# Kernel tuning notes

Hardware: AMD Instinct MI355X
Metric: run time of the kernel (lower is better)

Reference implementation:

```python
import jax, jax.numpy as jnp
import numpy as np

H = 1024  # hidden_dims

def _gru_scan(xs, h0, wih, whh, bih, bhh):
    # xs: (T, D_in); torch GRU gate order: r, z, n
    xp = xs @ wih.T + bih  # (T, 3H), precomputed input projection
    def step(h, xp_t):
        hh = h @ whh.T + bhh
        r = jax.nn.sigmoid(xp_t[:H] + hh[:H])
        z = jax.nn.sigmoid(xp_t[H:2 * H] + hh[H:2 * H])
        n = jnp.tanh(xp_t[2 * H:] + r * hh[2 * H:])
        h_new = (1.0 - z) * n + z * h
        return h_new, None
    h_last, _ = jax.lax.scan(step, h0, xp)
    return h_last

def _lstm_step(h_in, wih, bih, bhh):
    # single-step nn.LSTM(H, H) with zero initial (h0, c0): Whh terms vanish, biases remain.
    # torch LSTM gate order: i, f, g, o
    xp = h_in @ wih.T + bih + bhh  # (4H,)
    i = jax.nn.sigmoid(xp[:H])
    g = jnp.tanh(xp[2 * H:3 * H])
    o = jax.nn.sigmoid(xp[3 * H:])
    c = i * g  # f * c0 == 0
    return o * jnp.tanh(c)

def setup_inputs() -> dict:
    key = jax.random.key(0)
    ks = jax.random.split(key, 20)
    T, D_w, D_i = 8192, 32, 32
    s = 0.05
    inp = {
        "weather_window": jax.random.normal(ks[0], (T, 1, D_w), jnp.float32),
        "infect_window": jax.random.normal(ks[1], (T, 1, D_i), jnp.float32),
        "time_window": jax.random.uniform(ks[2], (T, 1), jnp.float32),
        "h_init": jax.random.normal(ks[3], (1, 1, H), jnp.float32),
        "enc_w1": jax.random.normal(ks[4], (512, 64), jnp.float32) * s,
        "enc_b1": jax.random.normal(ks[5], (512,), jnp.float32) * s,
        "enc_w2": jax.random.normal(ks[6], (1024, 512), jnp.float32) * s,
        "enc_b2": jax.random.normal(ks[7], (1024,), jnp.float32) * s,
        "gru_wih": jax.random.normal(ks[8], (3 * H, H), jnp.float32) * s,
        "gru_whh": jax.random.normal(ks[9], (3 * H, H), jnp.float32) * s,
        "gru_bih": jax.random.normal(ks[10], (3 * H,), jnp.float32) * s,
        "gru_bhh": jax.random.normal(ks[11], (3 * H,), jnp.float32) * s,
        "lstm_wih": jax.random.normal(ks[12], (4 * H, H), jnp.float32) * s,
        "lstm_bih": jax.random.normal(ks[13], (4 * H,), jnp.float32) * s,
        "lstm_bhh": jax.random.normal(ks[14], (4 * H,), jnp.float32) * s,
        "dec_w1": jax.random.normal(ks[15], (512, 1024), jnp.float32) * s,
        "dec_b1": jax.random.normal(ks[16], (512,), jnp.float32) * s,
        "dec_w2": jax.random.normal(ks[17], (8, 512), jnp.float32) * s,
        "dec_b2": jax.random.normal(ks[18], (8,), jnp.float32) * s,
    }
    return inp

def reference(weather_window, infect_window, time_window, h_init,
              enc_w1, enc_b1, enc_w2, enc_b2,
              gru_wih, gru_whh, gru_bih, gru_bhh,
              lstm_wih, lstm_bih, lstm_bhh,
              dec_w1, dec_b1, dec_w2, dec_b2):
    T = weather_window.shape[0]
    # use_diff_time = False branch
    data_window = jnp.concatenate([weather_window, infect_window], axis=2)  # (T,1,64)
    rev = data_window[::-1]  # flip(0)
    # Encoder FC stack
    x = jax.nn.relu(rev @ enc_w1.T + enc_b1)
    x = jax.nn.relu(x @ enc_w2.T + enc_b2)  # (T,1,H)
    # Encoder GRU -> final hidden state
    h_enc = _gru_scan(x[:, 0, :], h_init[0, 0], gru_wih, gru_whh, gru_bih, gru_bhh)  # (H,)
    def step(h, _):
        h_new = _lstm_step(h, lstm_wih, lstm_bih, lstm_bhh)
        return h_new, h_new
    _, hs_tail = jax.lax.scan(step, h_enc, None, length=T - 1)  # (T-1, H)
    hs = jnp.concatenate([h_enc[None, :], hs_tail], axis=0)  # (T, H)
    hs = hs[:, None, None, :]  # (T,1,1,H), matches torch.stack of (1,1,H)
    # Decoder FC stack
    y = jax.nn.relu(hs @ dec_w1.T + dec_b1)
    y = y @ dec_w2.T + dec_b2  # (T,1,1,8)
    return y
```

## Files before the change

kernel.cpp:

```cpp
#include <hip/hip_runtime.h>
#include <hip/hip_bf16.h>
#include <math.h>

#define T_STEPS 8192
#define HDIM    1024
#define GW      128
#define NSLOT   512

#define OFF_REV   ((size_t)0)
#define OFF_X1    ((size_t)2097152)
#define OFF_B     ((size_t)18874368)
#define OFF_C     ((size_t)52428800)
#define WS_NEEDED ((size_t)153092096)

typedef float f4 __attribute__((ext_vector_type(4)));

__device__ inline float sigm(float x)   { return 1.0f / (1.0f + __expf(-x)); }
__device__ inline float tanh_f(float x) { float e = __expf(2.0f * x); return 1.0f - 2.0f / (e + 1.0f); }

__device__ inline void store_cohr(f4* p, f4 v) {
    asm volatile("global_store_dwordx4 %0, %1, off sc0 sc1"
                 :: "v"(p), "v"(v) : "memory");
}

__device__ inline void poll_pair(const f4* p, unsigned want, f4& a, f4& b) {
    for (;;) {
        f4 va, vb;
        asm volatile("global_load_dwordx4 %0, %2, off sc0 sc1\n\t"
                     "global_load_dwordx4 %1, %2, off offset:16 sc0 sc1\n\t"
                     "s_waitcnt vmcnt(0)"
                     : "=&v"(va), "=&v"(vb) : "v"(p) : "memory");
        if (__float_as_uint(va.w) == want && __float_as_uint(vb.w) == want) {
            a = va; b = vb; return;
        }
        __builtin_amdgcn_s_sleep(1);
    }
}

__global__ void build_rev(const float* __restrict__ wea, const float* __restrict__ inf,
                          float* __restrict__ rev) {
    int idx = blockIdx.x * blockDim.x + threadIdx.x;
    if (idx >= T_STEPS * 64) return;
    int t = idx >> 6, c = idx & 63;
    int ts = T_STEPS - 1 - t;
    rev[idx] = (c < 32) ? wea[ts * 32 + c] : inf[ts * 32 + (c - 32)];
}

__global__ void seed_slots(const float* __restrict__ h0, f4* __restrict__ slots) {
    int i = blockIdx.x * blockDim.x + threadIdx.x;
    if (i < NSLOT) {
        f4 v;
        v.x = h0[2 * i]; v.y = h0[2 * i + 1]; v.z = 0.0f;
        v.w = __uint_as_float(0u);
        store_cohr(&slots[i], v);
    }
}

__global__ __launch_bounds__(256) void gemm_bias_act(
    const float* __restrict__ A, const float* __restrict__ W,
    const float* __restrict__ bias, float* __restrict__ C,
    int M, int N, int K, int relu)
{
    __shared__ float As[32][68];
    __shared__ float Ws[32][68];
    const int tid = threadIdx.x;
    const int tx = tid & 15, ty = tid >> 4;
    const int bm = blockIdx.y, bn = blockIdx.x;
    const float* Ab = A + (size_t)bm * 64 * K;
    const float* Wb = W + (size_t)bn * 64 * K;
    float acc[4][4] = {};

    for (int k0 = 0; k0 < K; k0 += 32) {
#pragma unroll
        for (int q = 0; q < 2; ++q) {
            int idx = tid * 2 + q;
            int row = idx >> 3;
            int kc  = (idx & 7) << 2;
            float4 av = *(const float4*)(Ab + (size_t)row * K + k0 + kc);
            As[kc + 0][row] = av.x; As[kc + 1][row] = av.y;
            As[kc + 2][row] = av.z; As[kc + 3][row] = av.w;
            float4 wv = *(const float4*)(Wb + (size_t)row * K + k0 + kc);
            Ws[kc + 0][row] = wv.x; Ws[kc + 1][row] = wv.y;
            Ws[kc + 2][row] = wv.z; Ws[kc + 3][row] = wv.w;
        }
        __syncthreads();
#pragma unroll
        for (int k = 0; k < 32; ++k) {
            float4 a = *(const float4*)&As[k][ty << 2];
            float4 b = *(const float4*)&Ws[k][tx << 2];
            acc[0][0] += a.x*b.x; acc[0][1] += a.x*b.y; acc[0][2] += a.x*b.z; acc[0][3] += a.x*b.w;
            acc[1][0] += a.y*b.x; acc[1][1] += a.y*b.y; acc[1][2] += a.y*b.z; acc[1][3] += a.y*b.w;
            acc[2][0] += a.z*b.x; acc[2][1] += a.z*b.y; acc[2][2] += a.z*b.z; acc[2][3] += a.z*b.w;
            acc[3][0] += a.w*b.x; acc[3][1] += a.w*b.y; acc[3][2] += a.w*b.z; acc[3][3] += a.w*b.w;
        }
        __syncthreads();
    }

    int m0 = bm * 64 + (ty << 2), n0 = bn * 64 + (tx << 2);
    float4 bv = *(const float4*)(bias + n0);
#pragma unroll
    for (int r = 0; r < 4; ++r) {
        float4 o;
        o.x = acc[r][0] + bv.x; o.y = acc[r][1] + bv.y;
        o.z = acc[r][2] + bv.z; o.w = acc[r][3] + bv.w;
        if (relu) {
            o.x = fmaxf(o.x, 0.f); o.y = fmaxf(o.y, 0.f);
            o.z = fmaxf(o.z, 0.f); o.w = fmaxf(o.w, 0.f);
        }
        *(float4*)(C + (size_t)(m0 + r) * N + n0) = o;
    }
}

__global__ __launch_bounds__(256, 1) void gru_scan(
    const float* __restrict__ whh,
    const float* __restrict__ bhh,
    const float* __restrict__ xp,
    f4* __restrict__ slots,
    float* __restrict__ hs)
{
    __shared__ float h_sh[2][HDIM];
    const int g = blockIdx.x, tid = threadIdx.x;
    const int w = tid >> 6, l = tid & 63;
    const int wv = g * 4 + w;
    const int iA = 2 * wv, iB = iA + 1;
    const int rows[6] = { iA, HDIM + iA, 2*HDIM + iA, iB, HDIM + iB, 2*HDIM + iB };

    f4 Wf[6][4];
#pragma unroll
    for (int r = 0; r < 6; ++r) {
        const float* wr = whh + (size_t)rows[r] * HDIM + 4 * l;
#pragma unroll
        for (int j = 0; j < 4; ++j) Wf[r][j] = *(const f4*)(wr + 256 * j);
    }
#pragma unroll
    for (int r = 0; r < 6; ++r)
#pragma unroll
        for (int j = 0; j < 4; ++j)
            asm volatile("" : "+v"(Wf[r][j]));

    float b0 = 0.f, b1 = 0.f, b2 = 0.f;
    float xv0 = 0.f, xv1 = 0.f, xv2 = 0.f;
    int xrow = (l == 0) ? iA : iB;
    if (l < 2) {
        b0 = bhh[xrow]; b1 = bhh[HDIM + xrow]; b2 = bhh[2*HDIM + xrow];
        xv0 = xp[xrow]; xv1 = xp[HDIM + xrow]; xv2 = xp[2*HDIM + xrow];
    }

    for (int t = 0; t < T_STEPS; ++t) {
        const int buf = t & 1;
        f4 sa, sb;
        poll_pair(slots + (size_t)buf * NSLOT + 2 * tid, (unsigned)t, sa, sb);
        h_sh[buf][4*tid + 0] = sa.x; h_sh[buf][4*tid + 1] = sa.y;
        h_sh[buf][4*tid + 2] = sb.x; h_sh[buf][4*tid + 3] = sb.y;
        __syncthreads();

        f4 h4[4];
#pragma unroll
        for (int j = 0; j < 4; ++j) h4[j] = *(const f4*)&h_sh[buf][256*j + 4*l];

        float red[6];
#pragma unroll
        for (int r = 0; r < 6; ++r) {
            f4 p = Wf[r][0]*h4[0] + Wf[r][1]*h4[1] + Wf[r][2]*h4[2] + Wf[r][3]*h4[3];
            float v = p.x + p.y + p.z + p.w;
#pragma unroll
            for (int off = 32; off > 0; off >>= 1) v += __shfl_xor(v, off, 64);
            red[r] = v;
        }

        float hn = 0.f;
        if (l < 2) {
            float rd0 = (l == 0) ? red[0] : red[3];
            float rd1 = (l == 0) ? red[1] : red[4];
            float rd2 = (l == 0) ? red[2] : red[5];
            float hh_r = rd0 + b0, hh_z = rd1 + b1, hh_n = rd2 + b2;
            float r_ = sigm(xv0 + hh_r);
            float z_ = sigm(xv1 + hh_z);
            float n_ = tanh_f(xv2 + r_ * hh_n);
            float hp = h_sh[buf][xrow];
            hn = (1.0f - z_) * n_ + z_ * hp;
        }
        float hBv = __shfl(hn, 1, 64);
        if (l == 0) {
            unsigned pub = (unsigned)(t + 1);
            f4 s; s.x = hn; s.y = hBv; s.z = 0.0f; s.w = __uint_as_float(pub);
            store_cohr(slots + (size_t)(pub & 1) * NSLOT + wv, s);
            if (t == T_STEPS - 1) { hs[iA] = hn; hs[iB] = hBv; }
        }
        if (l < 2 && t + 1 < T_STEPS) {
            const float* xq = xp + (size_t)(t + 1) * (3 * HDIM);
            xv0 = xq[xrow]; xv1 = xq[HDIM + xrow]; xv2 = xq[2*HDIM + xrow];
        }
    }
}

__global__ __launch_bounds__(256, 1) void lstm_scan(
    const float* __restrict__ wih,
    const float* __restrict__ bih,
    const float* __restrict__ bhh,
    f4* __restrict__ slots,
    float* __restrict__ hs)
{
    __shared__ float h_sh[2][HDIM];
    __shared__ int eqf[4];
    const int g = blockIdx.x, tid = threadIdx.x;
    const int w = tid >> 6, l = tid & 63;
    const int wv = g * 4 + w;
    const int iA = 2 * wv, iB = iA + 1;
    const int rows[6] = { iA, 2*HDIM + iA, 3*HDIM + iA, iB, 2*HDIM + iB, 3*HDIM + iB };

    f4 Wf[6][4];
#pragma unroll
    for (int r = 0; r < 6; ++r) {
        const float* wr = wih + (size_t)rows[r] * HDIM + 4 * l;
#pragma unroll
        for (int j = 0; j < 4; ++j) Wf[r][j] = *(const f4*)(wr + 256 * j);
    }
#pragma unroll
    for (int r = 0; r < 6; ++r)
#pragma unroll
        for (int j = 0; j < 4; ++j)
            asm volatile("" : "+v"(Wf[r][j]));

    float b0 = 0.f, b1 = 0.f, b2 = 0.f;
    int xrow = (l == 0) ? iA : iB;
    if (l < 2) {
        b0 = bih[xrow]          + bhh[xrow];
        b1 = bih[2*HDIM + xrow] + bhh[2*HDIM + xrow];
        b2 = bih[3*HDIM + xrow] + bhh[3*HDIM + xrow];
    }

    unsigned pax = 0u, pay = 0u, pbx = 0u, pby = 0u;

    for (int s = 1; s < T_STEPS; ++s) {
        const unsigned want = (unsigned)(8191 + s);
        const unsigned pub  = (unsigned)(8192 + s);
        const int buf = (int)(want & 1);
        f4 sa, sb;
        poll_pair(slots + (size_t)buf * NSLOT + 2 * tid, want, sa, sb);

        bool eq = (s > 1)
               && (__float_as_uint(sa.x) == pax) && (__float_as_uint(sa.y) == pay)
               && (__float_as_uint(sb.x) == pbx) && (__float_as_uint(sb.y) == pby);
        unsigned long long bm = __ballot(eq);
        if (l == 0) eqf[w] = (bm == ~0ull) ? 1 : 0;
        pax = __float_as_uint(sa.x); pay = __float_as_uint(sa.y);
        pbx = __float_as_uint(sb.x); pby = __float_as_uint(sb.y);

        h_sh[buf][4*tid + 0] = sa.x; h_sh[buf][4*tid + 1] = sa.y;
        h_sh[buf][4*tid + 2] = sb.x; h_sh[buf][4*tid + 3] = sb.y;
        __syncthreads();

        if (eqf[0] & eqf[1] & eqf[2] & eqf[3]) {
            float4 hv = make_float4(sa.x, sa.y, sb.x, sb.y);
            for (int k = s + g; k < T_STEPS; k += GW)
                *(float4*)&hs[(size_t)k * HDIM + 4 * tid] = hv;
            return;
        }

        f4 h4[4];
#pragma unroll
        for (int j = 0; j < 4; ++j) h4[j] = *(const f4*)&h_sh[buf][256*j + 4*l];

        float red[6];
#pragma unroll
        for (int r = 0; r < 6; ++r) {
            f4 p = Wf[r][0]*h4[0] + Wf[r][1]*h4[1] + Wf[r][2]*h4[2] + Wf[r][3]*h4[3];
            float v = p.x + p.y + p.z + p.w;
#pragma unroll
            for (int off = 32; off > 0; off >>= 1) v += __shfl_xor(v, off, 64);
            red[r] = v;
        }

        float hn = 0.f;
        if (l < 2) {
            float rd0 = (l == 0) ? red[0] : red[3];
            float rd1 = (l == 0) ? red[1] : red[4];
            float rd2 = (l == 0) ? red[2] : red[5];
            float i_ = sigm(rd0 + b0);
            float g_ = tanh_f(rd1 + b1);
            float o_ = sigm(rd2 + b2);
            hn = o_ * tanh_f(i_ * g_);
        }
        float hBv = __shfl(hn, 1, 64);
        if (l == 0) {
            f4 sv; sv.x = hn; sv.y = hBv; sv.z = 0.0f; sv.w = __uint_as_float(pub);
            store_cohr(slots + (size_t)(pub & 1) * NSLOT + wv, sv);
            hs[(size_t)s * HDIM + iA] = hn;
            hs[(size_t)s * HDIM + iB] = hBv;
        }
    }
}

__global__ __launch_bounds__(256) void dec2_kernel(
    const float* __restrict__ y1,
    const float* __restrict__ w2,
    const float* __restrict__ b2,
    float* __restrict__ out)
{
    const int w = threadIdx.x >> 6, l = threadIdx.x & 63;
    const int t = blockIdx.x * 4 + w;
    const float* yr = y1 + (size_t)t * 512;
    float yv[8];
#pragma unroll
    for (int j = 0; j < 8; ++j) yv[j] = yr[l + 64 * j];
    float o[8];
#pragma unroll
    for (int n = 0; n < 8; ++n) {
        const float* wr = w2 + n * 512;
        float s = 0.f;
#pragma unroll
        for (int j = 0; j < 8; ++j) s += yv[j] * wr[l + 64 * j];
#pragma unroll
        for (int off = 32; off > 0; off >>= 1) s += __shfl_xor(s, off, 64);
        o[n] = s;
    }
    if (l == 0) {
#pragma unroll
        for (int n = 0; n < 8; ++n) out[(size_t)t * 8 + n] = o[n] + b2[n];
    }
}

extern "C" void kernel_launch(void* const* d_in, const int* in_sizes, int n_in,
                              void* d_out, int out_size, void* d_ws, size_t ws_size,
                              hipStream_t stream)
{
    const float* wea      = (const float*)d_in[0];
    const float* inf      = (const float*)d_in[1];
    const float* h_init   = (const float*)d_in[3];
    const float* enc_w1   = (const float*)d_in[4];
    const float* enc_b1   = (const float*)d_in[5];
    const float* enc_w2   = (const float*)d_in[6];
    const float* enc_b2   = (const float*)d_in[7];
    const float* gru_wih  = (const float*)d_in[8];
    const float* gru_whh  = (const float*)d_in[9];
    const float* gru_bih  = (const float*)d_in[10];
    const float* gru_bhh  = (const float*)d_in[11];
    const float* lstm_wih = (const float*)d_in[12];
    const float* lstm_bih = (const float*)d_in[13];
    const float* lstm_bhh = (const float*)d_in[14];
    const float* dec_w1   = (const float*)d_in[15];
    const float* dec_b1   = (const float*)d_in[16];
    const float* dec_w2   = (const float*)d_in[17];
    const float* dec_b2   = (const float*)d_in[18];

    if (ws_size < WS_NEEDED) return;

    char* ws = (char*)d_ws;
    float* rev   = (float*)(ws + OFF_REV);
    float* x1    = (float*)(ws + OFF_X1);
    float* x2    = (float*)(ws + OFF_B);
    float* hs    = (float*)(ws + OFF_B);
    float* xp    = (float*)(ws + OFF_C);
    float* y1    = (float*)(ws + OFF_C);
    f4*    slots = (f4*)(ws + OFF_X1);

    build_rev<<<(T_STEPS * 64) / 256, 256, 0, stream>>>(wea, inf, rev);

    gemm_bias_act<<<dim3(8, 128), 256, 0, stream>>>(rev, enc_w1, enc_b1, x1,
                                                    T_STEPS, 512, 64, 1);
    gemm_bias_act<<<dim3(16, 128), 256, 0, stream>>>(x1, enc_w2, enc_b2, x2,
                                                     T_STEPS, 1024, 512, 1);
    gemm_bias_act<<<dim3(48, 128), 256, 0, stream>>>(x2, gru_wih, gru_bih, xp,
                                                     T_STEPS, 3 * HDIM, HDIM, 0);
    seed_slots<<<2, 256, 0, stream>>>(h_init, slots);
    gru_scan<<<GW, 256, 0, stream>>>(gru_whh, gru_bhh, xp, slots, hs);
    lstm_scan<<<GW, 256, 0, stream>>>(lstm_wih, lstm_bih, lstm_bhh, slots, hs);

    gemm_bias_act<<<dim3(8, 128), 256, 0, stream>>>(hs, dec_w1, dec_b1, y1,
                                                    T_STEPS, 512, HDIM, 1);
    dec2_kernel<<<T_STEPS / 4, 256, 0, stream>>>(y1, dec_w2, dec_b2, (float*)d_out);
}
```

Baseline: 43.09 ms.

## Detect periodic LSTM orbits with Brent-style anchors and replicate the cycle

The existing early exit only fires when the autoregressive hidden state becomes an exact fixed point. This change compares each new state against an anchor state that is reset at power-of-two steps, so an exact cycle of any period can be detected. Once a cycle is found, the remaining timesteps are filled by copying the earlier cycle entries from hs instead of running the serial recurrence. It also drops the s_sleep from the polling loop to cut per-step handoff latency. It writes hs with coherent stores and adds a fixed delay before the copy so other blocks' stores are visible. The cost is more spinning pressure on memory, plus reliance on those coherence assumptions when reading back hs.

```diff
diff --git a/kernel.cpp b/kernel.cpp
--- a/kernel.cpp
+++ b/kernel.cpp
@@ -14,12 +14,23 @@
 #define WS_NEEDED ((size_t)153092096)
 
 typedef float f4 __attribute__((ext_vector_type(4)));
+typedef float f2v __attribute__((ext_vector_type(2)));
 
 __device__ inline float sigm(float x)   { return 1.0f / (1.0f + __expf(-x)); }
 __device__ inline float tanh_f(float x) { float e = __expf(2.0f * x); return 1.0f - 2.0f / (e + 1.0f); }
 
+__device__ inline f4 load_cohr(const f4* p) {
+    f4 v;
+    asm volatile("global_load_dwordx4 %0, %1, off sc0 sc1\n\ts_waitcnt vmcnt(0)"
+                 : "=v"(v) : "v"(p) : "memory");
+    return v;
+}
 __device__ inline void store_cohr(f4* p, f4 v) {
     asm volatile("global_store_dwordx4 %0, %1, off sc0 sc1"
+                 :: "v"(p), "v"(v) : "memory");
+}
+__device__ inline void store_cohr8(f2v* p, f2v v) {
+    asm volatile("global_store_dwordx2 %0, %1, off sc0 sc1"
                  :: "v"(p), "v"(v) : "memory");
 }
 
@@ -33,7 +44,6 @@
         if (__float_as_uint(va.w) == want && __float_as_uint(vb.w) == want) {
             a = va; b = vb; return;
         }
-        __builtin_amdgcn_s_sleep(1);
     }
 }
 
@@ -230,7 +240,8 @@
         b2 = bih[3*HDIM + xrow] + bhh[3*HDIM + xrow];
     }
 
-    unsigned pax = 0u, pay = 0u, pbx = 0u, pby = 0u;
+    unsigned Rx = 0u, Ry = 0u, Rz = 0u, Rw = 0u;
+    int anchor = 0, npow = 1;
 
     for (int s = 1; s < T_STEPS; ++s) {
         const unsigned want = (unsigned)(8191 + s);
@@ -240,22 +251,35 @@
         poll_pair(slots + (size_t)buf * NSLOT + 2 * tid, want, sa, sb);
 
         bool eq = (s > 1)
-               && (__float_as_uint(sa.x) == pax) && (__float_as_uint(sa.y) == pay)
-               && (__float_as_uint(sb.x) == pbx) && (__float_as_uint(sb.y) == pby);
+               && (__float_as_uint(sa.x) == Rx) && (__float_as_uint(sa.y) == Ry)
+               && (__float_as_uint(sb.x) == Rz) && (__float_as_uint(sb.y) == Rw);
         unsigned long long bm = __ballot(eq);
         if (l == 0) eqf[w] = (bm == ~0ull) ? 1 : 0;
-        pax = __float_as_uint(sa.x); pay = __float_as_uint(sa.y);
-        pbx = __float_as_uint(sb.x); pby = __float_as_uint(sb.y);
 
         h_sh[buf][4*tid + 0] = sa.x; h_sh[buf][4*tid + 1] = sa.y;
         h_sh[buf][4*tid + 2] = sb.x; h_sh[buf][4*tid + 3] = sb.y;
         __syncthreads();
 
         if (eqf[0] & eqf[1] & eqf[2] & eqf[3]) {
-            float4 hv = make_float4(sa.x, sa.y, sb.x, sb.y);
-            for (int k = s + g; k < T_STEPS; k += GW)
-                *(float4*)&hs[(size_t)k * HDIM + 4 * tid] = hv;
+            const int p = (s - 1) - anchor;
+            for (int z = 0; z < 64; ++z) __builtin_amdgcn_s_sleep(8);
+            int k0 = s + g;
+            if (k0 < T_STEPS) {
+                int src = anchor + (k0 - anchor) % p;
+                const int stepmod = GW % p;
+                for (int k = k0; k < T_STEPS; k += GW) {
+                    f4 hv = load_cohr((const f4*)&hs[(size_t)src * HDIM + 4 * tid]);
+                    *(f4*)&hs[(size_t)k * HDIM + 4 * tid] = hv;
+                    src += stepmod; if (src >= anchor + p) src -= p;
+                }
+            }
             return;
+        }
+        if (s == 1 || s - 1 == npow) {
+            anchor = s - 1;
+            if (s > 1) npow <<= 1;
+            Rx = __float_as_uint(sa.x); Ry = __float_as_uint(sa.y);
+            Rz = __float_as_uint(sb.x); Rw = __float_as_uint(sb.y);
         }
 
         f4 h4[4];
@@ -286,8 +310,8 @@
         if (l == 0) {
             f4 sv; sv.x = hn; sv.y = hBv; sv.z = 0.0f; sv.w = __uint_as_float(pub);
             store_cohr(slots + (size_t)(pub & 1) * NSLOT + wv, sv);
-            hs[(size_t)s * HDIM + iA] = hn;
-            hs[(size_t)s * HDIM + iB] = hBv;
+            f2v hv2; hv2.x = hn; hv2.y = hBv;
+            store_cohr8((f2v*)&hs[(size_t)s * HDIM + iA], hv2);
         }
     }
 }
```

Measured after the change: 49.33 ms. 1.14x slower.
